# Kernel tuning notes

Hardware: AMD Instinct MI355X
Metric: run time of the kernel (lower is better)

Reference implementation:

```python
import jax, jax.numpy as jnp
import numpy as np

NUM_CLASSES = 80
SOFT_CENTER_RADIUS = 3.0
TOPK = 13
IOU_WEIGHT = 3.0
EPS = 1e-7
IOU_EPS = 1e-6
INF = 1e8


def _pairwise_iou(boxes, gts):
    # boxes: [B,N,4] xyxy, gts: [B,M,4] xyxy -> [B,N,M]
    lt = jnp.maximum(boxes[:, :, None, :2], gts[:, None, :, :2])
    rb = jnp.minimum(boxes[:, :, None, 2:], gts[:, None, :, 2:])
    wh = jnp.clip(rb - lt, 0.0)
    inter = wh[..., 0] * wh[..., 1]
    a1 = (boxes[..., 2] - boxes[..., 0]) * (boxes[..., 3] - boxes[..., 1])
    a2 = (gts[..., 2] - gts[..., 0]) * (gts[..., 3] - gts[..., 1])
    union = jnp.maximum(a1[:, :, None] + a2[:, None, :] - inter, IOU_EPS)
    return inter / union


def setup_inputs() -> dict:
    key = jax.random.key(0)
    ks = jax.random.split(key, 6)
    B, M, C, size = 32, 60, NUM_CLASSES, 640
    # grid priors for strides 8/16/32 -> N = 6400+1600+400 = 8400
    pr = []
    for s in (8, 16, 32):
        n = size // s
        ys, xs = jnp.meshgrid(jnp.arange(n) * s + s / 2.0,
                              jnp.arange(n) * s + s / 2.0, indexing='ij')
        pr.append(jnp.stack([xs.ravel(), ys.ravel(),
                             jnp.full((n * n,), float(s)),
                             jnp.full((n * n,), float(s))], -1))
    priors = jnp.concatenate(pr, 0).astype(jnp.float32)  # [8400,4]
    N = priors.shape[0]

    def make_boxes(k, b, m, wmin, wmax):
        c = jax.random.uniform(k, (b, m, 2), minval=0.0, maxval=float(size))
        wh = jax.random.uniform(jax.random.fold_in(k, 1), (b, m, 2),
                                minval=wmin, maxval=wmax)
        return jnp.concatenate([c - wh / 2, c + wh / 2], -1).astype(jnp.float32)

    pred_bboxes = make_boxes(ks[0], B, N, 5.0, 200.0)
    gt_bboxes = make_boxes(ks[1], B, M, 20.0, 200.0)
    pred_scores = (jax.random.normal(ks[2], (B, N, C)) * 2.0).astype(jnp.float32)
    gt_labels = jax.random.randint(ks[3], (B, M, 1), 0, C)
    nvalid = jax.random.randint(ks[4], (B,), 1, M + 1)
    pad_bbox_flag = (jnp.arange(M)[None, :] < nvalid[:, None]).astype(jnp.float32)[..., None]
    return dict(pred_bboxes=pred_bboxes, pred_scores=pred_scores, priors=priors,
                gt_labels=gt_labels, gt_bboxes=gt_bboxes, pad_bbox_flag=pad_bbox_flag)


def reference(pred_bboxes, pred_scores, priors, gt_labels, gt_bboxes, pad_bbox_flag):
    B, N, _ = pred_bboxes.shape
    M = gt_bboxes.shape[1]

    # --- inside-box mask (box_dim == 4) ---
    pc = priors[:, :2]  # [N,2]
    lt = pc[:, None, None] - gt_bboxes[..., :2]        # [N,B,M,2]
    rb = gt_bboxes[..., 2:] - pc[:, None, None]        # [N,B,M,2]
    is_in = jnp.min(jnp.concatenate([lt, rb], -1), -1) > 0  # [N,B,M]
    is_in = is_in * pad_bbox_flag[..., 0][None]        # mask padded gts
    is_in = jnp.transpose(is_in, (1, 0, 2))            # [B,N,M]
    valid_mask = is_in.sum(-1) > 0                     # [B,N]

    # --- soft center prior ---
    gt_center = (gt_bboxes[..., :2] + gt_bboxes[..., 2:]) / 2.0  # [B,M,2]
    strides = priors[:, 2]
    dist = jnp.sqrt(((pc[None, :, None, :] - gt_center[:, None, :, :]) ** 2).sum(-1)) \
        / strides[None, :, None]                       # [B,N,M]
    dist = dist * valid_mask[..., None]
    soft_center_prior = 10.0 ** (dist - SOFT_CENTER_RADIUS)

    # --- iou cost ---
    pairwise_ious = _pairwise_iou(pred_bboxes, gt_bboxes)  # [B,N,M]
    iou_cost = -jnp.log(pairwise_ious + EPS) * IOU_WEIGHT

    # --- cls cost: gather per-gt class logits ---
    labels = gt_labels[..., 0].astype(jnp.int32)        # [B,M]
    pw_logits = jnp.take_along_axis(
        pred_scores, jnp.broadcast_to(labels[:, None, :], (B, N, M)), axis=2)
    scale = pairwise_ious - jax.nn.sigmoid(pw_logits)
    bce = jnp.maximum(pw_logits, 0.0) - pw_logits * pairwise_ious \
        + jnp.log1p(jnp.exp(-jnp.abs(pw_logits)))       # stable BCE-with-logits
    cls_cost = bce * jnp.abs(scale) ** 2

    cost = cls_cost + iou_cost + soft_center_prior
    cost = jnp.where(valid_mask[..., None], cost, INF)

    # --- dynamic k matching ---
    k = min(TOPK, N)
    topk_ious = jax.lax.top_k(jnp.swapaxes(pairwise_ious, 1, 2), k)[0]  # [B,M,k]
    dynamic_ks = jnp.maximum(topk_ious.sum(-1).astype(jnp.int32), 1)    # [B,M]
    # rank of each prior within each gt column (ascending cost)
    rank = jnp.argsort(jnp.argsort(cost, axis=1), axis=1)               # [B,N,M]
    gt_valid = pad_bbox_flag[..., 0] > 0                                # [B,M]
    matching = (rank < dynamic_ks[:, None, :]) & gt_valid[:, None, :]   # [B,N,M] bool
    # resolve priors matched to >1 gt: keep min-cost gt
    multi = matching.sum(-1) > 1                                        # [B,N]
    amin = jnp.argmin(cost, axis=-1)                                    # [B,N]
    onehot = jnp.arange(M)[None, None, :] == amin[..., None]
    matching = jnp.where(multi[..., None], onehot, matching)
    fg_mask = matching.sum(-1) > 0                                      # [B,N]
    matched_gt_inds = jnp.argmax(matching, -1)                          # [B,N]
    matched_pred_ious = (matching * pairwise_ious).sum(-1)              # [B,N]

    # --- assemble outputs ---
    labels_g = jnp.take_along_axis(gt_labels[..., 0], matched_gt_inds, axis=1)
    assigned_labels = jnp.where(fg_mask, labels_g, NUM_CLASSES).astype(jnp.int32)
    assigned_labels_weights = jnp.ones((B, N), dtype=gt_bboxes.dtype)
    boxes_g = jnp.take_along_axis(gt_bboxes, matched_gt_inds[..., None], axis=1)
    assigned_bboxes = jnp.where(fg_mask[..., None], boxes_g, 0.0)
    assign_metrics = jnp.where(fg_mask, matched_pred_ious, 0.0)
    return (assigned_labels, assigned_labels_weights, assigned_bboxes, assign_metrics)
```

## Files before the change

### kernel.cpp

```cpp
#include <hip/hip_runtime.h>
#include <hip/hip_bf16.h>
#include <math.h>

#define B 32
#define N 8400
#define M 60
#define C 80
#define INF_COST 1e8f
#define NPART 4
#define PLEN 2100
#define PJ 9

typedef unsigned long long u64;

__device__ __forceinline__ float iou_fn(
    float px1, float py1, float px2, float py2,
    float gx1, float gy1, float gx2, float gy2)
{
#pragma clang fp contract(off)
    float ltx = fmaxf(px1, gx1), lty = fmaxf(py1, gy1);
    float rbx = fminf(px2, gx2), rby = fminf(py2, gy2);
    float wx = fmaxf(rbx - ltx, 0.0f), wy = fmaxf(rby - lty, 0.0f);
    float inter = wx * wy;
    float a1 = (px2 - px1) * (py2 - py1);
    float a2 = (gx2 - gx1) * (gy2 - gy1);
    float uni = fmaxf(a1 + a2 - inter, 1e-6f);
    return inter / uni;
}

__device__ __forceinline__ float cost_fast(
    float iou, float logit,
    float pcx, float pcy, float rstride,
    float gcx, float gcy)
{
#pragma clang fp contract(off)
    const float LOG2_10 = 3.3219280948873623f;
    const float LOG2_E  = 1.4426950408889634f;
    const float LN_2    = 0.6931471805599453f;
    float dx = pcx - gcx, dy = pcy - gcy;
    float dist = __builtin_amdgcn_sqrtf(dx * dx + dy * dy) * rstride;
    float soft = __builtin_amdgcn_exp2f((dist - 3.0f) * LOG2_10);
    float iouc = __builtin_amdgcn_logf(iou + 1e-7f) * (-3.0f * LN_2);
    float e    = __builtin_amdgcn_exp2f(-logit * LOG2_E);
    float sig  = __builtin_amdgcn_rcpf(1.0f + e);
    float t    = __builtin_amdgcn_exp2f(-fabsf(logit) * LOG2_E);
    float sp   = __builtin_amdgcn_logf(1.0f + t) * LN_2;
    float bce  = fmaxf(logit, 0.0f) - logit * iou + sp;
    float scale = iou - sig;
    float cls  = bce * scale * scale;
    return (cls + iouc) + soft;
}

__device__ __forceinline__ u64 wave_sort_asc(u64 key, int lane)
{
#pragma unroll
    for (int k = 2; k <= 64; k <<= 1) {
#pragma unroll
        for (int j = k >> 1; j > 0; j >>= 1) {
            u64 o = __shfl_xor((unsigned long long)key, j);
            bool keepmin = ((lane & k) == 0) == ((lane & j) == 0);
            bool take = (o < key) == keepmin;
            if (take) key = o;
        }
    }
    return key;
}

__global__ __launch_bounds__(256) void k_valid(
    const float* __restrict__ priors,
    const float* __restrict__ gt_bboxes,
    const float* __restrict__ pad,
    unsigned char* __restrict__ valid)
{
    int idx = blockIdx.x * 256 + threadIdx.x;
    if (idx >= B * N) return;
    int b = idx / N, n = idx % N;
    float px = priors[n * 4 + 0];
    float py = priors[n * 4 + 1];
    const float* g = gt_bboxes + (size_t)b * M * 4;
    const float* pf = pad + (size_t)b * M;
    unsigned char v = 0;
    for (int m = 0; m < M; m++) {
        float x1 = g[m * 4 + 0], y1 = g[m * 4 + 1];
        float x2 = g[m * 4 + 2], y2 = g[m * 4 + 3];
        float mn = fminf(fminf(px - x1, py - y1), fminf(x2 - px, y2 - py));
        if (mn > 0.0f && pf[m] > 0.0f) { v = 1; break; }
    }
    valid[idx] = v;
}

__global__ __launch_bounds__(256) void k_part(
    const float* __restrict__ pred_bboxes,
    const float* __restrict__ pred_scores,
    const float* __restrict__ priors,
    const int*   __restrict__ gt_labels,
    const float* __restrict__ gt_bboxes,
    const float* __restrict__ pad,
    const unsigned char* __restrict__ valid,
    float* __restrict__ PI, float* __restrict__ PC, int* __restrict__ PN)
{
    __shared__ u64      s_ckey[4][13];
    __shared__ u64      s_ikey[4][13];
    __shared__ u64      s_thr[2];
    __shared__ float    s_cv[160]; __shared__ int s_cn[160];
    __shared__ float    s_iv[160]; __shared__ int s_in[160];
    __shared__ unsigned s_cnt[2];
    __shared__ float    s_slotc[13]; __shared__ int s_slotn[13];
    __shared__ float    s_sloti[13];

    const int i = blockIdx.x;
    const int bm = i >> 2, part = i & 3;
    if (pad[bm] == 0.0f) return;

    const int b = bm / M;
    const int tid = threadIdx.x;
    const int lane = tid & 63;
    const int w = tid >> 6;
    const int base = part * PLEN;

    if (tid == 0) { s_cnt[0] = 0; s_cnt[1] = 0; }

    const float4 g = ((const float4*)gt_bboxes)[bm];
    const float gx1 = g.x, gy1 = g.y, gx2 = g.z, gy2 = g.w;
    const float gcx = (gx1 + gx2) * 0.5f, gcy = (gy1 + gy2) * 0.5f;
    const int label = gt_labels[bm];
    const float4* pb4 = ((const float4*)pred_bboxes) + (size_t)b * N;
    const float* srow = pred_scores + (size_t)b * N * C;
    const unsigned char* vrow = valid + (size_t)b * N;
    const float4* pr4 = (const float4*)priors;

    float myi[PJ], myc[PJ], lg[PJ];
    unsigned vmask = 0;
    u64 minc = ~0ull, maxi = ~0ull;

#pragma unroll
    for (int j = 0; j < PJ; ++j) {
        int off = tid + (j << 8);
        float v = 0.0f, l = 0.0f;
        if (off < PLEN) {
            int n = base + off;
            float4 p = pb4[n];
            v = iou_fn(p.x, p.y, p.z, p.w, gx1, gy1, gx2, gy2);
            u64 ik = ((u64)(0xFFFFFFFFu - __float_as_uint(v)) << 32) | (unsigned)n;
            if (ik < maxi) maxi = ik;
            if (vrow[n]) {
                vmask |= (1u << j);
                l = srow[(size_t)n * C + label];
            }
        }
        myi[j] = v; lg[j] = l;
    }

#pragma unroll
    for (int j = 0; j < PJ; ++j) {
        int off = tid + (j << 8);
        float c = 0.0f;
        if (off < PLEN) {
            int n = base + off;
            if (vmask & (1u << j)) {
                float4 pr = pr4[n];
                c = cost_fast(myi[j], lg[j], pr.x, pr.y,
                              __builtin_amdgcn_rcpf(pr.z), gcx, gcy);
            } else c = INF_COST;
            u64 ck = ((u64)__float_as_uint(c) << 32) | (unsigned)n;
            if (ck < minc) minc = ck;
        }
        myc[j] = c;
    }

    {
        u64 sc = wave_sort_asc(minc, lane);
        if (lane < 13) s_ckey[w][lane] = sc;
        u64 si = wave_sort_asc(maxi, lane);
        if (lane < 13) s_ikey[w][lane] = si;
    }
    __syncthreads();

    if (tid < 2) {
        const u64 (*L)[13] = (tid == 0) ? s_ckey : s_ikey;
        int q0 = 0, q1 = 0, q2 = 0, q3 = 0;
        u64 t = 0;
        for (int r = 0; r < 13; ++r) {
            u64 v0 = L[0][q0], v1 = L[1][q1], v2 = L[2][q2], v3 = L[3][q3];
            u64 bv = v0; int bw = 0;
            if (v1 < bv) { bv = v1; bw = 1; }
            if (v2 < bv) { bv = v2; bw = 2; }
            if (v3 < bv) { bv = v3; bw = 3; }
            t = bv;
            if (bw == 0) q0++; else if (bw == 1) q1++; else if (bw == 2) q2++; else q3++;
        }
        s_thr[tid] = t;
    }
    __syncthreads();
    const u64 tc = s_thr[0];
    const u64 ti = s_thr[1];

#pragma unroll
    for (int j = 0; j < PJ; ++j) {
        int off = tid + (j << 8);
        if (off < PLEN) {
            int n = base + off;
            u64 ck = ((u64)__float_as_uint(myc[j]) << 32) | (unsigned)n;
            if (ck <= tc) {
                unsigned p = atomicAdd(&s_cnt[0], 1u);
                if (p < 160u) { s_cv[p] = myc[j]; s_cn[p] = n; }
            }
            u64 ik = ((u64)(0xFFFFFFFFu - __float_as_uint(myi[j])) << 32) | (unsigned)n;
            if (ik <= ti) {
                unsigned p = atomicAdd(&s_cnt[1], 1u);
                if (p < 160u) { s_iv[p] = myi[j]; s_in[p] = n; }
            }
        }
    }
    __syncthreads();

    {
        const unsigned nc = s_cnt[0], ng = s_cnt[1];
        if (tid < 128) {
            unsigned ii = tid;
            if (ii < nc) {
                float c = s_cv[ii]; int nn = s_cn[ii];
                unsigned r = 0;
                for (unsigned t = 0; t < nc; ++t) {
                    float u = s_cv[t];
                    r += (u < c || (u == c && s_cn[t] < nn)) ? 1u : 0u;
                }
                if (r < 13u) { s_slotc[r] = c; s_slotn[r] = nn; }
            }
        } else {
            unsigned ii = tid - 128;
            if (ii < ng) {
                float v = s_iv[ii]; int nn = s_in[ii];
                unsigned r = 0;
                for (unsigned t = 0; t < ng; ++t) {
                    float u = s_iv[t];
                    r += (u > v || (u == v && s_in[t] < nn)) ? 1u : 0u;
                }
                if (r < 13u) s_sloti[r] = v;
            }
        }
    }
    __syncthreads();

    if (tid < 13) {
        int o = (bm * NPART + part) * 13 + tid;
        PC[o] = s_slotc[tid];
        PN[o] = s_slotn[tid];
        PI[o] = s_sloti[tid];
    }
}

__global__ __launch_bounds__(256) void k_merge(
    const float* __restrict__ pad,
    const float* __restrict__ PI,
    const float* __restrict__ PC,
    const int*   __restrict__ PN,
    float* __restrict__ cK, int* __restrict__ nK)
{
    int bm = blockIdx.x * 256 + threadIdx.x;
    if (bm >= B * M) return;
    if (pad[bm] == 0.0f) return;

    const float* pi = PI + (size_t)bm * 52;
    const float* pc = PC + (size_t)bm * 52;
    const int*   pn = PN + (size_t)bm * 52;

    int q0 = 0, q1 = 0, q2 = 0, q3 = 0;
    float ss = 0.0f;
    for (int r = 0; r < 13; ++r) {
        float v0 = (q0 < 13) ? pi[q0]      : -1.0f;
        float v1 = (q1 < 13) ? pi[13 + q1] : -1.0f;
        float v2 = (q2 < 13) ? pi[26 + q2] : -1.0f;
        float v3 = (q3 < 13) ? pi[39 + q3] : -1.0f;
        float bv = v0; int bw = 0;
        if (v1 > bv) { bv = v1; bw = 1; }
        if (v2 > bv) { bv = v2; bw = 2; }
        if (v3 > bv) { bv = v3; bw = 3; }
        ss += bv;
        if (bw == 0) q0++; else if (bw == 1) q1++; else if (bw == 2) q2++; else q3++;
    }
    int K = (int)ss;
    if (K < 1) K = 1;

    q0 = q1 = q2 = q3 = 0;
    float ck = 0.0f; int nk = 0;
    for (int r = 0; r < K; ++r) {
        float c0 = (q0 < 13) ? pc[q0]      : INFINITY; int n0 = (q0 < 13) ? pn[q0]      : 0x7fffffff;
        float c1 = (q1 < 13) ? pc[13 + q1] : INFINITY; int n1 = (q1 < 13) ? pn[13 + q1] : 0x7fffffff;
        float c2 = (q2 < 13) ? pc[26 + q2] : INFINITY; int n2 = (q2 < 13) ? pn[26 + q2] : 0x7fffffff;
        float c3 = (q3 < 13) ? pc[39 + q3] : INFINITY; int n3 = (q3 < 13) ? pn[39 + q3] : 0x7fffffff;
        float bv = c0; int bn = n0, bw = 0;
        if (c1 < bv || (c1 == bv && n1 < bn)) { bv = c1; bn = n1; bw = 1; }
        if (c2 < bv || (c2 == bv && n2 < bn)) { bv = c2; bn = n2; bw = 2; }
        if (c3 < bv || (c3 == bv && n3 < bn)) { bv = c3; bn = n3; bw = 3; }
        ck = bv; nk = bn;
        if (bw == 0) q0++; else if (bw == 1) q1++; else if (bw == 2) q2++; else q3++;
    }
    cK[bm] = ck; nK[bm] = nk;
}

__global__ __launch_bounds__(256) void k_assign(
    const float* __restrict__ pred_bboxes,
    const float* __restrict__ pred_scores,
    const float* __restrict__ priors,
    const int*   __restrict__ gt_labels,
    const float* __restrict__ gt_bboxes,
    const float* __restrict__ pad,
    const unsigned char* __restrict__ valid,
    const float* __restrict__ cK,
    const int*   __restrict__ nK,
    float* __restrict__ out)
{
    __shared__ float s_box[M][4];
    __shared__ float s_gc[M][2];
    __shared__ float s_ck[M];
    __shared__ int   s_lab[M];
    __shared__ int   s_nk[M];
    __shared__ unsigned char s_gtv[M];

    const int cidx = blockIdx.x;
    const int b = cidx / 33;
    const int chunk = cidx % 33;
    const int n = chunk * 256 + threadIdx.x;

    if (threadIdx.x < M) {
        int m = threadIdx.x, gi = b * M + m;
        float4 g = ((const float4*)gt_bboxes)[gi];
        s_box[m][0] = g.x; s_box[m][1] = g.y; s_box[m][2] = g.z; s_box[m][3] = g.w;
        s_gc[m][0] = (g.x + g.z) * 0.5f;
        s_gc[m][1] = (g.y + g.w) * 0.5f;
        s_ck[m] = cK[gi];
        s_lab[m] = gt_labels[gi];
        s_nk[m] = nK[gi];
        s_gtv[m] = (pad[gi] > 0.0f) ? 1 : 0;
    }
    __syncthreads();
    if (n >= N) return;

    const size_t idx = (size_t)b * N + n;
    const float4 p = ((const float4*)pred_bboxes)[idx];
    const int vn = valid[idx];

    float* o_lab = out;
    float* o_w   = out + (size_t)B * N;
    float* o_box = out + (size_t)2 * B * N;
    float* o_met = out + (size_t)6 * B * N;

    int count = 0, firstm = -1;
    int mstar; float mi;

    if (!vn) {
#pragma unroll
        for (int m = 0; m < M; m++) {
            float ckm = s_ck[m]; int nkm = s_nk[m];
            bool matched = s_gtv[m] &&
                           (INF_COST < ckm || (INF_COST == ckm && n <= nkm));
            if (matched) { count++; if (firstm < 0) firstm = m; }
        }
        mstar = (count > 1) ? 0 : firstm;
        mi = 0.0f;
        if (mstar >= 0)
            mi = iou_fn(p.x, p.y, p.z, p.w,
                        s_box[mstar][0], s_box[mstar][1], s_box[mstar][2], s_box[mstar][3]);
    } else {
        const float4 pr = ((const float4*)priors)[n];
        const float rst = __builtin_amdgcn_rcpf(pr.z);
        const float* scores = pred_scores + idx * C;

        float minc = INFINITY; int amin = 0;
        float firstiou = 0.0f, aminiou = 0.0f;

        for (int mc = 0; mc < 4; ++mc) {
            float lg[15];
#pragma unroll
            for (int t = 0; t < 15; ++t) lg[t] = scores[s_lab[mc * 15 + t]];
#pragma unroll
            for (int t = 0; t < 15; ++t) {
                int m = mc * 15 + t;
                float iou = iou_fn(p.x, p.y, p.z, p.w,
                                   s_box[m][0], s_box[m][1], s_box[m][2], s_box[m][3]);
                float c = cost_fast(iou, lg[t], pr.x, pr.y, rst, s_gc[m][0], s_gc[m][1]);
                if (c < minc) { minc = c; amin = m; aminiou = iou; }
                float ckm = s_ck[m]; int nkm = s_nk[m];
                bool matched = s_gtv[m] && (c < ckm || (c == ckm && n <= nkm));
                if (matched) { count++; if (firstm < 0) { firstm = m; firstiou = iou; } }
            }
        }
        if (count > 1)       { mstar = amin;   mi = aminiou; }
        else if (count == 1) { mstar = firstm; mi = firstiou; }
        else                 { mstar = -1;     mi = 0.0f; }
    }

    o_w[idx] = 1.0f;
    if (mstar >= 0) {
        o_lab[idx] = (float)s_lab[mstar];
        o_box[idx * 4 + 0] = s_box[mstar][0];
        o_box[idx * 4 + 1] = s_box[mstar][1];
        o_box[idx * 4 + 2] = s_box[mstar][2];
        o_box[idx * 4 + 3] = s_box[mstar][3];
        o_met[idx] = mi;
    } else {
        o_lab[idx] = (float)C;
        o_box[idx * 4 + 0] = 0.0f;
        o_box[idx * 4 + 1] = 0.0f;
        o_box[idx * 4 + 2] = 0.0f;
        o_box[idx * 4 + 3] = 0.0f;
        o_met[idx] = 0.0f;
    }
}

extern "C" void kernel_launch(void* const* d_in, const int* in_sizes, int n_in,
                              void* d_out, int out_size, void* d_ws, size_t ws_size,
                              hipStream_t stream) {
    const float* pred_bboxes = (const float*)d_in[0];
    const float* pred_scores = (const float*)d_in[1];
    const float* priors      = (const float*)d_in[2];
    const int*   gt_labels   = (const int*)d_in[3];
    const float* gt_bboxes   = (const float*)d_in[4];
    const float* pad         = (const float*)d_in[5];
    float* out = (float*)d_out;

    unsigned char* ws = (unsigned char*)d_ws;
    size_t off = 0;
    unsigned char* valid = ws;                  off += (size_t)B * N;
    float* cKp = (float*)(ws + off);            off += (size_t)B * M * 4;
    int*   nKp = (int*)(ws + off);              off += (size_t)B * M * 4;
    float* PI  = (float*)(ws + off);            off += (size_t)B * M * NPART * 13 * 4;
    float* PC  = (float*)(ws + off);            off += (size_t)B * M * NPART * 13 * 4;
    int*   PN  = (int*)(ws + off);              off += (size_t)B * M * NPART * 13 * 4;

    k_valid<<<(B * N + 255) / 256, 256, 0, stream>>>(priors, gt_bboxes, pad, valid);
    k_part <<<B * M * NPART, 256, 0, stream>>>(pred_bboxes, pred_scores, priors, gt_labels,
                                               gt_bboxes, pad, valid, PI, PC, PN);
    k_merge<<<(B * M + 255) / 256, 256, 0, stream>>>(pad, PI, PC, PN, cKp, nKp);
    k_assign<<<33 * B, 256, 0, stream>>>(pred_bboxes, pred_scores, priors, gt_labels,
                                         gt_bboxes, pad, valid, cKp, nKp, out);
}
```

Baseline: 144.4 us.

## Prune cost evaluation with lower-bound filter before gathering class logits

Computes a cheap lower bound on cost (IoU and center terms only, since the BCE class term is non-negative), selects the 13 smallest bounds, evaluates the full cost for those to get a threshold, and then computes the full cost only for priors whose bound is below that threshold. The aim is to skip most strided gathers from the large score tensor and the sigmoid/softplus math. In exchange it adds extra sort and merge passes and more block synchronisations. Correctness depends on the bound being valid and on the sentinel handling.

New measurement: 149.8 us. 1.04x slower.

```diff
diff --git a/kernel.cpp b/kernel.cpp
--- a/kernel.cpp
+++ b/kernel.cpp
@@ -7,6 +7,7 @@
 #define M 60
 #define C 80
 #define INF_COST 1e8f
+#define SENTINEL 1e30f
 #define NPART 4
 #define PLEN 2100
 #define PJ 9
@@ -51,6 +52,19 @@
     return (cls + iouc) + soft;
 }
 
+__device__ __forceinline__ float lb_fast(
+    float iou, float pcx, float pcy, float rstride, float gcx, float gcy)
+{
+#pragma clang fp contract(off)
+    const float LOG2_10 = 3.3219280948873623f;
+    const float LN_2    = 0.6931471805599453f;
+    float dx = pcx - gcx, dy = pcy - gcy;
+    float dist = __builtin_amdgcn_sqrtf(dx * dx + dy * dy) * rstride;
+    float soft = __builtin_amdgcn_exp2f((dist - 3.0f) * LOG2_10);
+    float iouc = __builtin_amdgcn_logf(iou + 1e-7f) * (-3.0f * LN_2);
+    return iouc + soft;
+}
+
 __device__ __forceinline__ u64 wave_sort_asc(u64 key, int lane)
 {
 #pragma unroll
@@ -99,7 +113,7 @@
     const unsigned char* __restrict__ valid,
     float* __restrict__ PI, float* __restrict__ PC, int* __restrict__ PN)
 {
-    __shared__ u64      s_ckey[4][13];
+    __shared__ u64      s_k1[4][13];
     __shared__ u64      s_ikey[4][13];
     __shared__ u64      s_thr[2];
     __shared__ float    s_cv[160]; __shared__ int s_cn[160];
@@ -107,6 +121,8 @@
     __shared__ unsigned s_cnt[2];
     __shared__ float    s_slotc[13]; __shared__ int s_slotn[13];
     __shared__ float    s_sloti[13];
+    __shared__ float    s_exc[13];
+    __shared__ float    s_T;
 
     const int i = blockIdx.x;
     const int bm = i >> 2, part = i & 3;
@@ -129,14 +145,14 @@
     const unsigned char* vrow = valid + (size_t)b * N;
     const float4* pr4 = (const float4*)priors;
 
-    float myi[PJ], myc[PJ], lg[PJ];
+    float myi[PJ], mylb[PJ], myc[PJ];
     unsigned vmask = 0;
-    u64 minc = ~0ull, maxi = ~0ull;
+    u64 minlb = ~0ull, maxi = ~0ull;
 
 #pragma unroll
     for (int j = 0; j < PJ; ++j) {
         int off = tid + (j << 8);
-        float v = 0.0f, l = 0.0f;
+        float v = 0.0f, lb = 0.0f;
         if (off < PLEN) {
             int n = base + off;
             float4 p = pb4[n];
@@ -145,39 +161,25 @@
             if (ik < maxi) maxi = ik;
             if (vrow[n]) {
                 vmask |= (1u << j);
-                l = srow[(size_t)n * C + label];
-            }
-        }
-        myi[j] = v; lg[j] = l;
-    }
-
-#pragma unroll
-    for (int j = 0; j < PJ; ++j) {
-        int off = tid + (j << 8);
-        float c = 0.0f;
-        if (off < PLEN) {
-            int n = base + off;
-            if (vmask & (1u << j)) {
                 float4 pr = pr4[n];
-                c = cost_fast(myi[j], lg[j], pr.x, pr.y,
-                              __builtin_amdgcn_rcpf(pr.z), gcx, gcy);
-            } else c = INF_COST;
-            u64 ck = ((u64)__float_as_uint(c) << 32) | (unsigned)n;
-            if (ck < minc) minc = ck;
-        }
-        myc[j] = c;
+                lb = lb_fast(v, pr.x, pr.y, __builtin_amdgcn_rcpf(pr.z), gcx, gcy);
+            } else lb = INF_COST;
+            u64 lk = ((u64)__float_as_uint(lb) << 32) | (unsigned)n;
+            if (lk < minlb) minlb = lk;
+        }
+        myi[j] = v; mylb[j] = lb;
     }
 
     {
-        u64 sc = wave_sort_asc(minc, lane);
-        if (lane < 13) s_ckey[w][lane] = sc;
+        u64 sc = wave_sort_asc(minlb, lane);
+        if (lane < 13) s_k1[w][lane] = sc;
         u64 si = wave_sort_asc(maxi, lane);
         if (lane < 13) s_ikey[w][lane] = si;
     }
     __syncthreads();
 
     if (tid < 2) {
-        const u64 (*L)[13] = (tid == 0) ? s_ckey : s_ikey;
+        const u64 (*L)[13] = (tid == 0) ? s_k1 : s_ikey;
         int q0 = 0, q1 = 0, q2 = 0, q3 = 0;
         u64 t = 0;
         for (int r = 0; r < 13; ++r) {
@@ -192,18 +194,18 @@
         s_thr[tid] = t;
     }
     __syncthreads();
-    const u64 tc = s_thr[0];
-    const u64 ti = s_thr[1];
+    const u64 tlb = s_thr[0];
+    const u64 ti  = s_thr[1];
 
 #pragma unroll
     for (int j = 0; j < PJ; ++j) {
         int off = tid + (j << 8);
         if (off < PLEN) {
             int n = base + off;
-            u64 ck = ((u64)__float_as_uint(myc[j]) << 32) | (unsigned)n;
-            if (ck <= tc) {
+            u64 lk = ((u64)__float_as_uint(mylb[j]) << 32) | (unsigned)n;
+            if (lk <= tlb) {
                 unsigned p = atomicAdd(&s_cnt[0], 1u);
-                if (p < 160u) { s_cv[p] = myc[j]; s_cn[p] = n; }
+                if (p < 160u) { s_cv[p] = mylb[j]; s_cn[p] = n; }
             }
             u64 ik = ((u64)(0xFFFFFFFFu - __float_as_uint(myi[j])) << 32) | (unsigned)n;
             if (ik <= ti) {
@@ -238,6 +240,103 @@
                 }
                 if (r < 13u) s_sloti[r] = v;
             }
+        }
+    }
+    __syncthreads();
+
+    if (tid < 13) {
+        int n = s_slotn[tid];
+        float c;
+        if (vrow[n]) {
+            float4 p = pb4[n];
+            float v = iou_fn(p.x, p.y, p.z, p.w, gx1, gy1, gx2, gy2);
+            float4 pr = pr4[n];
+            float logit = srow[(size_t)n * C + label];
+            c = cost_fast(v, logit, pr.x, pr.y, __builtin_amdgcn_rcpf(pr.z), gcx, gcy);
+        } else {
+            c = INF_COST;
+        }
+        s_exc[tid] = c;
+    }
+    __syncthreads();
+    if (tid == 0) {
+        float T = s_exc[0];
+        for (int a = 1; a < 13; ++a) T = fmaxf(T, s_exc[a]);
+        s_T = T;
+        s_cnt[0] = 0;
+    }
+    __syncthreads();
+    const float T = s_T;
+
+    u64 minc = ~0ull;
+#pragma unroll
+    for (int j = 0; j < PJ; ++j) {
+        int off = tid + (j << 8);
+        float c = 0.0f;
+        if (off < PLEN) {
+            int n = base + off;
+            if (!(vmask & (1u << j))) {
+                c = INF_COST;
+            } else if (mylb[j] > T) {
+                c = SENTINEL;
+            } else {
+                float4 pr = pr4[n];
+                float logit = srow[(size_t)n * C + label];
+                c = cost_fast(myi[j], logit, pr.x, pr.y,
+                              __builtin_amdgcn_rcpf(pr.z), gcx, gcy);
+            }
+            u64 ck = ((u64)__float_as_uint(c) << 32) | (unsigned)n;
+            if (ck < minc) minc = ck;
+        }
+        myc[j] = c;
+    }
+
+    {
+        u64 sc = wave_sort_asc(minc, lane);
+        if (lane < 13) s_k1[w][lane] = sc;
+    }
+    __syncthreads();
+    if (tid == 0) {
+        int q0 = 0, q1 = 0, q2 = 0, q3 = 0;
+        u64 t = 0;
+        for (int r = 0; r < 13; ++r) {
+            u64 v0 = s_k1[0][q0], v1 = s_k1[1][q1], v2 = s_k1[2][q2], v3 = s_k1[3][q3];
+            u64 bv = v0; int bw = 0;
+            if (v1 < bv) { bv = v1; bw = 1; }
+            if (v2 < bv) { bv = v2; bw = 2; }
+            if (v3 < bv) { bv = v3; bw = 3; }
+            t = bv;
+            if (bw == 0) q0++; else if (bw == 1) q1++; else if (bw == 2) q2++; else q3++;
+        }
+        s_thr[0] = t;
+    }
+    __syncthreads();
+    const u64 tc = s_thr[0];
+
+#pragma unroll
+    for (int j = 0; j < PJ; ++j) {
+        int off = tid + (j << 8);
+        if (off < PLEN) {
+            int n = base + off;
+            u64 ck = ((u64)__float_as_uint(myc[j]) << 32) | (unsigned)n;
+            if (ck <= tc) {
+                unsigned p = atomicAdd(&s_cnt[0], 1u);
+                if (p < 160u) { s_cv[p] = myc[j]; s_cn[p] = n; }
+            }
+        }
+    }
+    __syncthreads();
+
+    {
+        const unsigned nc = s_cnt[0];
+        for (unsigned ii = tid; ii < nc; ii += 256) {
+            float c = s_cv[ii]; int nn = s_cn[ii];
+            unsigned r = 0;
+            for (unsigned t = 0; t < nc; ++t) {
+                float u = s_cv[t];
+                r += (u < c || (u == c && s_cn[t] < nn)) ? 1u : 0u;
+            }
+            if (r < 13u) { s_slotc[r] = c; s_slotn[r] = nn; }
         }
     }
     __syncthreads();
```
